# Performance work log

Hardware: AMD Instinct MI355X
Metric: run time of the kernel (lower is better)

The kernel has to match this reference:

```python
import jax, jax.numpy as jnp
import numpy as np

NUM_EMB = 8192
DIM = 64
DECAY = 0.99
EPS = 1e-05
COMMIT = 0.25


def setup_inputs() -> dict:
    key = jax.random.key(0)
    k1, k2, k3 = jax.random.split(key, 3)
    inputs = jax.random.normal(k1, (8, 4096, DIM), jnp.float32)
    weight = jax.random.normal(k2, (NUM_EMB, DIM), jnp.float32)
    ema_cluster_count = jnp.ones((NUM_EMB,), jnp.float32)
    ema_weight_sum = jax.random.normal(k3, (NUM_EMB, DIM), jnp.float32)
    return {
        'inputs': inputs,
        'weight': weight,
        'ema_cluster_count': ema_cluster_count,
        'ema_weight_sum': ema_weight_sum,
    }


def reference(inputs, weight, ema_cluster_count, ema_weight_sum):
    flat = inputs.reshape(-1, DIM)  # [N, D]
    distances = (
        jnp.sum(flat ** 2, axis=1, keepdims=True)
        + jnp.sum(weight ** 2, axis=1)
        - 2.0 * flat @ weight.T
    )
    idx = jnp.argmin(distances, axis=1)  # [N] int

    # EMA stats (training branch): one-hot column sums == segment counts,
    # encodings.T @ flat == segment sums of inputs by code index.
    counts = jax.ops.segment_sum(
        jnp.ones(flat.shape[0], jnp.float32), idx, num_segments=NUM_EMB)
    new_cc = ema_cluster_count * DECAY + (1.0 - DECAY) * counts
    emb_sum = jax.ops.segment_sum(flat, idx, num_segments=NUM_EMB)
    new_ws = ema_weight_sum * DECAY + (1.0 - DECAY) * emb_sum

    n = jnp.sum(new_cc)
    smoothed = (new_cc + EPS) / (n + NUM_EMB * EPS) * n
    new_weight = new_ws / smoothed[:, None]  # updated codebook [K, D]

    quantized_raw = new_weight[idx].reshape(inputs.shape)
    e_latent_loss = jnp.mean((jax.lax.stop_gradient(quantized_raw) - inputs) ** 2)
    vq_loss = COMMIT * e_latent_loss

    avg_probs = counts / flat.shape[0]
    perplexity = jnp.exp(-jnp.sum(avg_probs * jnp.log(avg_probs + 1e-10)))

    # straight-through estimator
    quantized = inputs + jax.lax.stop_gradient(quantized_raw - inputs)
    return quantized, vq_loss, idx, perplexity, new_weight, new_cc, new_ws
```

## Files before the change

kernel.cpp:

```cpp
#include <hip/hip_runtime.h>
#include <math.h>

typedef _Float16 f16x8 __attribute__((ext_vector_type(8)));
typedef float f32x4 __attribute__((ext_vector_type(4)));

#define NROWS 32768
#define KEMB  8192

#define DECAYF 0.99f
#define OMDF   0.01f

#define OUT_Q    0
#define OUT_LOSS 2097152
#define OUT_IDX  2097153
#define OUT_PERP 2129921
#define OUT_NW   2129922
#define OUT_NCC  2654210
#define OUT_NWS  2662402

#define WS_N      0
#define WS_ENT    1
#define WS_COUNTS 4
#define WS_EMB    8196
#define WS_IDX    532484
#define WS_W2H    565252
#define WS_WFRAG  573444
#define WS_ZERO_UNITS 532484

__device__ __forceinline__ float sq_rn(float v) { return __fmul_rn(v, v); }

__device__ __forceinline__ float npsumsq64(const float* vbuf) {
  float a[8];
#pragma unroll
  for (int j = 0; j < 8; ++j) a[j] = sq_rn(vbuf[j]);
#pragma unroll
  for (int m = 1; m < 8; ++m)
#pragma unroll
    for (int j = 0; j < 8; ++j) a[j] = __fadd_rn(a[j], sq_rn(vbuf[m*8 + j]));
  return __fadd_rn(__fadd_rn(__fadd_rn(a[0],a[1]), __fadd_rn(a[2],a[3])),
                   __fadd_rn(__fadd_rn(a[4],a[5]), __fadd_rn(a[6],a[7])));
}

__device__ __forceinline__ void split_f16(float x, _Float16& hi, _Float16& lo) {
  hi = (_Float16)x;
  float r = __fsub_rn(x, (float)hi);
  lo = (_Float16)r;
}

__global__ __launch_bounds__(256) void prep_kernel(const float* __restrict__ wg,
                                                   float* __restrict__ ws) {
  const int tid = blockIdx.x * 256 + threadIdx.x;
  if (tid < KEMB) {
    const float* src = wg + (size_t)tid * 64;
    float vbuf[64];
#pragma unroll
    for (int f = 0; f < 16; ++f) {
      float4 v = *(const float4*)(src + f*4);
      vbuf[f*4+0]=v.x; vbuf[f*4+1]=v.y; vbuf[f*4+2]=v.z; vbuf[f*4+3]=v.w;
    }
    ws[WS_W2H + tid] = __fmul_rn(0.5f, npsumsq64(vbuf));
  } else if (tid < KEMB + 65536) {
    const int u = tid - KEMB;
    const int K = u >> 3, g = u & 7;
    const int n = K & 15, P = K >> 4;
    const int slot = (g&3)*16 + n, shi = g >> 2;
    const float* src = wg + (size_t)K*64 + g*8;
    float4 v0 = *(const float4*)src, v1 = *(const float4*)(src + 4);
    float vv[8] = {v0.x,v0.y,v0.z,v0.w,v1.x,v1.y,v1.z,v1.w};
    f16x8 hi, lo;
#pragma unroll
    for (int j = 0; j < 8; ++j) { _Float16 h, l; split_f16(vv[j], h, l); hi[j]=h; lo[j]=l; }
    _Float16* wf = (_Float16*)(ws + WS_WFRAG);
    *(f16x8*)&wf[((size_t)(P*4 + shi)*64 + slot)*8]     = hi;
    *(f16x8*)&wf[((size_t)(P*4 + 2 + shi)*64 + slot)*8] = lo;
  }
}

#define COMPUTE_PANEL(I, B0, B1, B2, B3, W2)                                        \
  {                                                                                 \
    const f32x4 cin = {(W2), (W2), (W2), (W2)};                                     \
    f32x4 acc[2];                                                                   \
    _Pragma("unroll")                                                               \
    for (int rt = 0; rt < 2; ++rt) acc[rt] = __builtin_amdgcn_mfma_f32_16x16x32_f16(a[rt][0], (B0), cin, 0,0,0); \
    _Pragma("unroll")                                                               \
    for (int rt = 0; rt < 2; ++rt) acc[rt] = __builtin_amdgcn_mfma_f32_16x16x32_f16(a[rt][1], (B1), acc[rt], 0,0,0); \
    _Pragma("unroll")                                                               \
    for (int rt = 0; rt < 2; ++rt) acc[rt] = __builtin_amdgcn_mfma_f32_16x16x32_f16(a[rt][2], (B0), acc[rt], 0,0,0); \
    _Pragma("unroll")                                                               \
    for (int rt = 0; rt < 2; ++rt) acc[rt] = __builtin_amdgcn_mfma_f32_16x16x32_f16(a[rt][3], (B1), acc[rt], 0,0,0); \
    _Pragma("unroll")                                                               \
    for (int rt = 0; rt < 2; ++rt) acc[rt] = __builtin_amdgcn_mfma_f32_16x16x32_f16(a[rt][0], (B2), acc[rt], 0,0,0); \
    _Pragma("unroll")                                                               \
    for (int rt = 0; rt < 2; ++rt) acc[rt] = __builtin_amdgcn_mfma_f32_16x16x32_f16(a[rt][1], (B3), acc[rt], 0,0,0); \
    const int kk = (I)*64 + cg*16 + n16;                                            \
    _Pragma("unroll")                                                               \
    for (int rt = 0; rt < 2; ++rt)                                                  \
      _Pragma("unroll")                                                             \
      for (int reg = 0; reg < 4; ++reg) {                                           \
        const float dist = acc[rt][reg];                                            \
        const int bi = rt*4 + reg;                                                  \
        if (dist < best[bi]) { best[bi] = dist; bestk[bi] = kk; }                   \
      }                                                                             \
  }

#define LOADB(I, C0, C1, C2, C3, CW)                                                \
  {                                                                                 \
    const size_t base = ((size_t)((I)*4 + cg) * 256) * 8 + lane8;                   \
    C0 = *(const f16x8*)&wfrag[base];                                               \
    C1 = *(const f16x8*)&wfrag[base + 512];                                         \
    C2 = *(const f16x8*)&wfrag[base + 1024];                                        \
    C3 = *(const f16x8*)&wfrag[base + 1536];                                        \
    CW = w2hg[(I)*64 + cg*16 + n16];                                                \
  }

__global__ __launch_bounds__(1024) void argmin_kernel(const float* __restrict__ xg,
                                                      float* __restrict__ out,
                                                      float* __restrict__ ws) {
  __shared__ __align__(16) _Float16 xp[8*4*64*8];
  __shared__ float md[128*4];
  __shared__ int   mk[128*4];
  __shared__ int   bkL[128];

  const int t    = threadIdx.x;
  const int lane = t & 63, wv = t >> 6;
  const int quad = lane >> 4, n16 = lane & 15;
  const int rg = wv >> 2, cg = wv & 3;
  const int row0 = blockIdx.x * 128;
  const _Float16* __restrict__ wfrag = (const _Float16*)(ws + WS_WFRAG);
  const float* __restrict__ w2hg = ws + WS_W2H;

  {
    const int u  = t;
    const int rp = u >> 7, n = (u >> 3) & 15, g = u & 7;
    const float* src = xg + (size_t)(row0 + rp*16 + n)*64 + g*8;
    float4 v0 = *(const float4*)src, v1 = *(const float4*)(src + 4);
    float vv[8] = {v0.x,v0.y,v0.z,v0.w,v1.x,v1.y,v1.z,v1.w};
    f16x8 hi, lo;
#pragma unroll
    for (int j = 0; j < 8; ++j) { _Float16 h, l; split_f16(-vv[j], h, l); hi[j]=h; lo[j]=l; }
    const int slot = (g&3)*16 + n, shi = g >> 2;
    *(f16x8*)&xp[(((rp*4) + shi)*64 + slot)*8]     = hi;
    *(f16x8*)&xp[(((rp*4) + 2 + shi)*64 + slot)*8] = lo;
  }
  __syncthreads();

  f16x8 a[2][4];
#pragma unroll
  for (int rt = 0; rt < 2; ++rt)
#pragma unroll
    for (int s = 0; s < 4; ++s)
      a[rt][s] = *(const f16x8*)&xp[(((rg*2+rt)*4 + s)*64 + lane)*8];

  float best[8]; int bestk[8];
#pragma unroll
  for (int i = 0; i < 8; ++i) { best[i] = INFINITY; bestk[i] = 0; }

  const size_t lane8 = (size_t)lane * 8;
  f16x8 p0, p1, p2, p3, q0, q1, q2, q3;
  float pw, qw;
  LOADB(0, p0, p1, p2, p3, pw);

  for (int it = 0; it < 128; it += 2) {
    LOADB(it+1, q0, q1, q2, q3, qw);
    COMPUTE_PANEL(it, p0, p1, p2, p3, pw);
    if (it + 2 < 128) LOADB(it+2, p0, p1, p2, p3, pw);
    COMPUTE_PANEL(it+1, q0, q1, q2, q3, qw);
  }

#pragma unroll
  for (int bi = 0; bi < 8; ++bi) {
    float bd = best[bi]; int bk = bestk[bi];
#pragma unroll
    for (int m = 1; m < 16; m <<= 1) {
      const float od = __shfl_xor(bd, m, 64);
      const int   ok = __shfl_xor(bk, m, 64);
      if (od < bd || (od == bd && ok < bk)) { bd = od; bk = ok; }
    }
    best[bi] = bd; bestk[bi] = bk;
  }
  if (n16 == 0) {
#pragma unroll
    for (int rt = 0; rt < 2; ++rt)
#pragma unroll
      for (int reg = 0; reg < 4; ++reg) {
        const int row = rg*32 + rt*16 + quad*4 + reg;
        md[row*4 + cg] = best[rt*4+reg];
        mk[row*4 + cg] = bestk[rt*4+reg];
      }
  }
  __syncthreads();

  if (t < 128) {
    const int row = t;
    float bd = md[row*4]; int bk = mk[row*4];
#pragma unroll
    for (int u = 1; u < 4; ++u) {
      const float d2 = md[row*4 + u]; const int k2 = mk[row*4 + u];
      if (d2 < bd || (d2 == bd && k2 < bk)) { bd = d2; bk = k2; }
    }
    out[OUT_IDX + row0 + row] = (float)bk;
    ((int*)ws)[WS_IDX + row0 + row] = bk;
    bkL[row] = bk;
    atomicAdd(&ws[WS_COUNTS + bk], 1.0f);
  }
  __syncthreads();

#pragma unroll 4
  for (int r = 0; r < 8; ++r) {
    const int row = wv*8 + r;
    const int k = bkL[row];
    atomicAdd(&ws[WS_EMB + (size_t)k*64 + lane],
              xg[(size_t)(row0 + row)*64 + lane]);
  }
}

__global__ __launch_bounds__(256) void stats_kernel(const float* __restrict__ cc,
                                                    float* __restrict__ out,
                                                    float* __restrict__ ws) {
  const int t = threadIdx.x;
  float v1 = 0.0f, v2 = 0.0f;
#pragma unroll
  for (int i = 0; i < 32; ++i) {
    const int k = i*256 + t;
    const float cnt = ws[WS_COUNTS + k];
    const float ncc = __fadd_rn(__fmul_rn(DECAYF, cc[k]), __fmul_rn(OMDF, cnt));
    out[OUT_NCC + k] = ncc;
    const float p = cnt * (1.0f/32768.0f);
    v1 += ncc;
    v2 += __fmul_rn(p, logf(__fadd_rn(p, 1e-10f)));
  }
#pragma unroll
  for (int off = 32; off > 0; off >>= 1) {
    v1 += __shfl_down(v1, off);
    v2 += __shfl_down(v2, off);
  }
  __shared__ float s1[4], s2[4];
  const int lane = t & 63, wid = t >> 6;
  if (lane == 0) { s1[wid] = v1; s2[wid] = v2; }
  __syncthreads();
  if (t == 0) {
    ws[WS_N]   = (s1[0]+s1[1]) + (s1[2]+s1[3]);
    ws[WS_ENT] = (s2[0]+s2[1]) + (s2[2]+s2[3]);
  }
}

__global__ __launch_bounds__(256) void update_kernel(const float* __restrict__ ws0,
                                                     float* __restrict__ out,
                                                     float* __restrict__ ws) {
  const int e4 = blockIdx.x * 256 + threadIdx.x;
  const int k = e4 >> 4;
  const float n = ws[WS_N];
  const float ncc = out[OUT_NCC + k];
  const float smoothed = __fmul_rn(__fadd_rn(ncc, 1e-5f) / __fadd_rn(n, 0.08192f), n);
  float4 w0 = *(const float4*)(ws0 + (size_t)e4*4);
  float4 em = *(const float4*)(ws + WS_EMB + (size_t)e4*4);
  float wv[4] = {w0.x, w0.y, w0.z, w0.w};
  float ev[4] = {em.x, em.y, em.z, em.w};
  float nwsv[4], nwv[4];
#pragma unroll
  for (int i = 0; i < 4; ++i) {
    nwsv[i] = __fadd_rn(__fmul_rn(DECAYF, wv[i]), __fmul_rn(OMDF, ev[i]));
    nwv[i]  = nwsv[i] / smoothed;
  }
  float4 onws = {nwsv[0], nwsv[1], nwsv[2], nwsv[3]};
  float4 onw  = {nwv[0],  nwv[1],  nwv[2],  nwv[3]};
  *(float4*)(out + OUT_NWS + (size_t)e4*4) = onws;
  *(float4*)(out + OUT_NW  + (size_t)e4*4) = onw;
  if (e4 == 0) out[OUT_PERP] = expf(-ws[WS_ENT]);
}

__global__ __launch_bounds__(256) void quant_kernel(const float* __restrict__ xg,
                                                    float* __restrict__ out,
                                                    float* __restrict__ ws) {
  const int t = threadIdx.x;
  const int* idxb = (const int*)ws + WS_IDX;
  float v = 0.0f;
#pragma unroll
  for (int j = 0; j < 4; ++j) {
    const int e4 = (j*512 + blockIdx.x)*256 + t;
    const int row = e4 >> 4, d = (e4 & 15) * 4;
    const int k = idxb[row];
    const float* nw = out + OUT_NW + (size_t)k*64 + d;
    float2 q0 = *(const float2*)nw, q1 = *(const float2*)(nw + 2);
    float4 x = *(const float4*)(xg + (size_t)e4*4);
    float qv[4] = {q0.x, q0.y, q1.x, q1.y};
    float xv[4] = {x.x, x.y, x.z, x.w};
    float4 o;
    float ov[4];
#pragma unroll
    for (int i = 0; i < 4; ++i) {
      const float df = __fsub_rn(qv[i], xv[i]);
      ov[i] = __fadd_rn(xv[i], df);
      v = fmaf(df, df, v);
    }
    o.x = ov[0]; o.y = ov[1]; o.z = ov[2]; o.w = ov[3];
    *(float4*)(out + OUT_Q + (size_t)e4*4) = o;
  }
#pragma unroll
  for (int off = 32; off > 0; off >>= 1) v += __shfl_down(v, off);
  __shared__ float sm[4];
  const int lane = t & 63, wid = t >> 6;
  if (lane == 0) sm[wid] = v;
  __syncthreads();
  if (t == 0) ws[WS_COUNTS + blockIdx.x] = (sm[0]+sm[1]) + (sm[2]+sm[3]);
}

__global__ void final_kernel(float* __restrict__ out, const float* __restrict__ ws) {
  const int t = threadIdx.x;
  float v = 0.0f;
#pragma unroll
  for (int i = 0; i < 8; ++i) v += ws[WS_COUNTS + i*64 + t];
#pragma unroll
  for (int off = 32; off > 0; off >>= 1) v += __shfl_down(v, off);
  if (t == 0) out[OUT_LOSS] = __fmul_rn(0.25f, v / 2097152.0f);
}

extern "C" void kernel_launch(void* const* d_in, const int* in_sizes, int n_in,
                              void* d_out, int out_size, void* d_ws, size_t ws_size,
                              hipStream_t stream) {
  (void)in_sizes; (void)n_in; (void)out_size; (void)ws_size;
  const float* x   = (const float*)d_in[0];
  const float* w   = (const float*)d_in[1];
  const float* cc  = (const float*)d_in[2];
  const float* ws0 = (const float*)d_in[3];
  float* out = (float*)d_out;
  float* ws  = (float*)d_ws;

  hipMemsetAsync(d_ws, 0, (size_t)WS_ZERO_UNITS * 4, stream);
  hipLaunchKernelGGL(prep_kernel,   dim3(288),  dim3(256),  0, stream, w, ws);
  hipLaunchKernelGGL(argmin_kernel, dim3(256),  dim3(1024), 0, stream, x, out, ws);
  hipLaunchKernelGGL(stats_kernel,  dim3(1),    dim3(256),  0, stream, cc, out, ws);
  hipLaunchKernelGGL(update_kernel, dim3(512),  dim3(256),  0, stream, ws0, out, ws);
  hipLaunchKernelGGL(quant_kernel,  dim3(512),  dim3(256),  0, stream, x, out, ws);
  hipLaunchKernelGGL(final_kernel,  dim3(1),    dim3(64),   0, stream, out, ws);
}
```

Before: 202.9 us.

## Switch argmin to 32x32x16 MFMA tiles with 512-thread blocks, fold memset into prep

Reorganizes the codebook and input fragment layouts for 32x32x16 f16 MFMA. Each wave now computes 64 rows by 32 codes per panel, with 8-wave blocks and two blocks per CU. This reduces B-fragment loads and per-instruction overhead relative to the 16x16 tiles. The workspace memset is folded into prep_kernel to remove a separate launch, and stats_kernel uses 1024 threads. More accumulator and best/bestk registers per thread raise register pressure.

```diff
diff --git a/kernel.cpp b/kernel.cpp
--- a/kernel.cpp
+++ b/kernel.cpp
@@ -3,6 +3,7 @@
 
 typedef _Float16 f16x8 __attribute__((ext_vector_type(8)));
 typedef float f32x4 __attribute__((ext_vector_type(4)));
+typedef float f32x16 __attribute__((ext_vector_type(16)));
 
 #define NROWS 32768
 #define KEMB  8192
@@ -50,6 +51,7 @@
 __global__ __launch_bounds__(256) void prep_kernel(const float* __restrict__ wg,
                                                    float* __restrict__ ws) {
   const int tid = blockIdx.x * 256 + threadIdx.x;
+  for (int i = tid; i < WS_ZERO_UNITS; i += 73728) ws[i] = 0.0f;
   if (tid < KEMB) {
     const float* src = wg + (size_t)tid * 64;
     float vbuf[64];
@@ -59,133 +61,148 @@
       vbuf[f*4+0]=v.x; vbuf[f*4+1]=v.y; vbuf[f*4+2]=v.z; vbuf[f*4+3]=v.w;
     }
     ws[WS_W2H + tid] = __fmul_rn(0.5f, npsumsq64(vbuf));
-  } else if (tid < KEMB + 65536) {
+  } else {
     const int u = tid - KEMB;
     const int K = u >> 3, g = u & 7;
-    const int n = K & 15, P = K >> 4;
-    const int slot = (g&3)*16 + n, shi = g >> 2;
+    const int P = K >> 5, col = K & 31;
+    const int c = g >> 1, h = g & 1;
+    const int lane_t = col + 32*h;
     const float* src = wg + (size_t)K*64 + g*8;
     float4 v0 = *(const float4*)src, v1 = *(const float4*)(src + 4);
     float vv[8] = {v0.x,v0.y,v0.z,v0.w,v1.x,v1.y,v1.z,v1.w};
     f16x8 hi, lo;
 #pragma unroll
-    for (int j = 0; j < 8; ++j) { _Float16 h, l; split_f16(vv[j], h, l); hi[j]=h; lo[j]=l; }
+    for (int j = 0; j < 8; ++j) { _Float16 hh, ll; split_f16(vv[j], hh, ll); hi[j]=hh; lo[j]=ll; }
     _Float16* wf = (_Float16*)(ws + WS_WFRAG);
-    *(f16x8*)&wf[((size_t)(P*4 + shi)*64 + slot)*8]     = hi;
-    *(f16x8*)&wf[((size_t)(P*4 + 2 + shi)*64 + slot)*8] = lo;
-  }
-}
-
-#define COMPUTE_PANEL(I, B0, B1, B2, B3, W2)                                        \
-  {                                                                                 \
-    const f32x4 cin = {(W2), (W2), (W2), (W2)};                                     \
-    f32x4 acc[2];                                                                   \
-    _Pragma("unroll")                                                               \
-    for (int rt = 0; rt < 2; ++rt) acc[rt] = __builtin_amdgcn_mfma_f32_16x16x32_f16(a[rt][0], (B0), cin, 0,0,0); \
-    _Pragma("unroll")                                                               \
-    for (int rt = 0; rt < 2; ++rt) acc[rt] = __builtin_amdgcn_mfma_f32_16x16x32_f16(a[rt][1], (B1), acc[rt], 0,0,0); \
-    _Pragma("unroll")                                                               \
-    for (int rt = 0; rt < 2; ++rt) acc[rt] = __builtin_amdgcn_mfma_f32_16x16x32_f16(a[rt][2], (B0), acc[rt], 0,0,0); \
-    _Pragma("unroll")                                                               \
-    for (int rt = 0; rt < 2; ++rt) acc[rt] = __builtin_amdgcn_mfma_f32_16x16x32_f16(a[rt][3], (B1), acc[rt], 0,0,0); \
-    _Pragma("unroll")                                                               \
-    for (int rt = 0; rt < 2; ++rt) acc[rt] = __builtin_amdgcn_mfma_f32_16x16x32_f16(a[rt][0], (B2), acc[rt], 0,0,0); \
-    _Pragma("unroll")                                                               \
-    for (int rt = 0; rt < 2; ++rt) acc[rt] = __builtin_amdgcn_mfma_f32_16x16x32_f16(a[rt][1], (B3), acc[rt], 0,0,0); \
-    const int kk = (I)*64 + cg*16 + n16;                                            \
-    _Pragma("unroll")                                                               \
-    for (int rt = 0; rt < 2; ++rt)                                                  \
-      _Pragma("unroll")                                                             \
-      for (int reg = 0; reg < 4; ++reg) {                                           \
-        const float dist = acc[rt][reg];                                            \
-        const int bi = rt*4 + reg;                                                  \
-        if (dist < best[bi]) { best[bi] = dist; bestk[bi] = kk; }                   \
-      }                                                                             \
-  }
-
-#define LOADB(I, C0, C1, C2, C3, CW)                                                \
-  {                                                                                 \
-    const size_t base = ((size_t)((I)*4 + cg) * 256) * 8 + lane8;                   \
-    C0 = *(const f16x8*)&wfrag[base];                                               \
-    C1 = *(const f16x8*)&wfrag[base + 512];                                         \
-    C2 = *(const f16x8*)&wfrag[base + 1024];                                        \
-    C3 = *(const f16x8*)&wfrag[base + 1536];                                        \
-    CW = w2hg[(I)*64 + cg*16 + n16];                                                \
-  }
-
-__global__ __launch_bounds__(1024) void argmin_kernel(const float* __restrict__ xg,
-                                                      float* __restrict__ out,
-                                                      float* __restrict__ ws) {
-  __shared__ __align__(16) _Float16 xp[8*4*64*8];
+    *(f16x8*)&wf[((size_t)(P*8 + c)    *64 + lane_t)*8] = hi;
+    *(f16x8*)&wf[((size_t)(P*8 + c + 4)*64 + lane_t)*8] = lo;
+  }
+}
+
+__global__ __launch_bounds__(512, 2) void argmin_kernel(const float* __restrict__ xg,
+                                                        float* __restrict__ out,
+                                                        float* __restrict__ ws) {
+  __shared__ __align__(16) _Float16 xp[4*8*64*8];
   __shared__ float md[128*4];
   __shared__ int   mk[128*4];
   __shared__ int   bkL[128];
 
   const int t    = threadIdx.x;
   const int lane = t & 63, wv = t >> 6;
-  const int quad = lane >> 4, n16 = lane & 15;
+  const int col = lane & 31, half = lane >> 5;
   const int rg = wv >> 2, cg = wv & 3;
   const int row0 = blockIdx.x * 128;
   const _Float16* __restrict__ wfrag = (const _Float16*)(ws + WS_WFRAG);
   const float* __restrict__ w2hg = ws + WS_W2H;
 
-  {
-    const int u  = t;
-    const int rp = u >> 7, n = (u >> 3) & 15, g = u & 7;
-    const float* src = xg + (size_t)(row0 + rp*16 + n)*64 + g*8;
+#pragma unroll
+  for (int it = 0; it < 2; ++it) {
+    const int u  = t + 512*it;
+    const int r = u >> 3, g = u & 7;
+    const int rp = r >> 5, c = g >> 1, h = g & 1;
+    const int lane_t = (r & 31) + 32*h;
+    const float* src = xg + (size_t)(row0 + r)*64 + g*8;
     float4 v0 = *(const float4*)src, v1 = *(const float4*)(src + 4);
     float vv[8] = {v0.x,v0.y,v0.z,v0.w,v1.x,v1.y,v1.z,v1.w};
     f16x8 hi, lo;
 #pragma unroll
-    for (int j = 0; j < 8; ++j) { _Float16 h, l; split_f16(-vv[j], h, l); hi[j]=h; lo[j]=l; }
-    const int slot = (g&3)*16 + n, shi = g >> 2;
-    *(f16x8*)&xp[(((rp*4) + shi)*64 + slot)*8]     = hi;
-    *(f16x8*)&xp[(((rp*4) + 2 + shi)*64 + slot)*8] = lo;
-  }
-  __syncthreads();
-
-  f16x8 a[2][4];
+    for (int j = 0; j < 8; ++j) { _Float16 hh, ll; split_f16(-vv[j], hh, ll); hi[j]=hh; lo[j]=ll; }
+    *(f16x8*)&xp[(((rp*8) + c)    *64 + lane_t)*8] = hi;
+    *(f16x8*)&xp[(((rp*8) + c + 4)*64 + lane_t)*8] = lo;
+  }
+  __syncthreads();
+
+  f16x8 a[2][8];
 #pragma unroll
   for (int rt = 0; rt < 2; ++rt)
 #pragma unroll
-    for (int s = 0; s < 4; ++s)
-      a[rt][s] = *(const f16x8*)&xp[(((rg*2+rt)*4 + s)*64 + lane)*8];
-
-  float best[8]; int bestk[8];
-#pragma unroll
-  for (int i = 0; i < 8; ++i) { best[i] = INFINITY; bestk[i] = 0; }
+    for (int c = 0; c < 8; ++c)
+      a[rt][c] = *(const f16x8*)&xp[(((rg*2+rt)*8 + c)*64 + lane)*8];
+
+  float best[32]; int bestk[32];
+#pragma unroll
+  for (int i = 0; i < 32; ++i) { best[i] = INFINITY; bestk[i] = 0; }
 
   const size_t lane8 = (size_t)lane * 8;
-  f16x8 p0, p1, p2, p3, q0, q1, q2, q3;
+
+#define LOADB32(P, B, CW)                                                    \
+  {                                                                          \
+    const size_t base = (size_t)(P)*4096 + lane8;                            \
+    _Pragma("unroll")                                                        \
+    for (int c = 0; c < 8; ++c) B[c] = *(const f16x8*)&wfrag[base + c*512];  \
+    CW = w2hg[(P)*32 + col];                                                 \
+  }
+
+#define COMPUTE32(P, B, W2)                                                  \
+  {                                                                          \
+    f32x16 cin;                                                              \
+    _Pragma("unroll")                                                        \
+    for (int i = 0; i < 16; ++i) cin[i] = (W2);                              \
+    f32x16 ac0, ac1;                                                         \
+    ac0 = __builtin_amdgcn_mfma_f32_32x32x16_f16(a[0][0], B[0], cin, 0,0,0); \
+    ac1 = __builtin_amdgcn_mfma_f32_32x32x16_f16(a[1][0], B[0], cin, 0,0,0); \
+    ac0 = __builtin_amdgcn_mfma_f32_32x32x16_f16(a[0][1], B[1], ac0, 0,0,0); \
+    ac1 = __builtin_amdgcn_mfma_f32_32x32x16_f16(a[1][1], B[1], ac1, 0,0,0); \
+    ac0 = __builtin_amdgcn_mfma_f32_32x32x16_f16(a[0][2], B[2], ac0, 0,0,0); \
+    ac1 = __builtin_amdgcn_mfma_f32_32x32x16_f16(a[1][2], B[2], ac1, 0,0,0); \
+    ac0 = __builtin_amdgcn_mfma_f32_32x32x16_f16(a[0][3], B[3], ac0, 0,0,0); \
+    ac1 = __builtin_amdgcn_mfma_f32_32x32x16_f16(a[1][3], B[3], ac1, 0,0,0); \
+    ac0 = __builtin_amdgcn_mfma_f32_32x32x16_f16(a[0][0], B[4], ac0, 0,0,0); \
+    ac1 = __builtin_amdgcn_mfma_f32_32x32x16_f16(a[1][0], B[4], ac1, 0,0,0); \
+    ac0 = __builtin_amdgcn_mfma_f32_32x32x16_f16(a[0][1], B[5], ac0, 0,0,0); \
+    ac1 = __builtin_amdgcn_mfma_f32_32x32x16_f16(a[1][1], B[5], ac1, 0,0,0); \
+    ac0 = __builtin_amdgcn_mfma_f32_32x32x16_f16(a[0][2], B[6], ac0, 0,0,0); \
+    ac1 = __builtin_amdgcn_mfma_f32_32x32x16_f16(a[1][2], B[6], ac1, 0,0,0); \
+    ac0 = __builtin_amdgcn_mfma_f32_32x32x16_f16(a[0][3], B[7], ac0, 0,0,0); \
+    ac1 = __builtin_amdgcn_mfma_f32_32x32x16_f16(a[1][3], B[7], ac1, 0,0,0); \
+    ac0 = __builtin_amdgcn_mfma_f32_32x32x16_f16(a[0][4], B[0], ac0, 0,0,0); \
+    ac1 = __builtin_amdgcn_mfma_f32_32x32x16_f16(a[1][4], B[0], ac1, 0,0,0); \
+    ac0 = __builtin_amdgcn_mfma_f32_32x32x16_f16(a[0][5], B[1], ac0, 0,0,0); \
+    ac1 = __builtin_amdgcn_mfma_f32_32x32x16_f16(a[1][5], B[1], ac1, 0,0,0); \
+    ac0 = __builtin_amdgcn_mfma_f32_32x32x16_f16(a[0][6], B[2], ac0, 0,0,0); \
+    ac1 = __builtin_amdgcn_mfma_f32_32x32x16_f16(a[1][6], B[2], ac1, 0,0,0); \
+    ac0 = __builtin_amdgcn_mfma_f32_32x32x16_f16(a[0][7], B[3], ac0, 0,0,0); \
+    ac1 = __builtin_amdgcn_mfma_f32_32x32x16_f16(a[1][7], B[3], ac1, 0,0,0); \
+    const int kk = (P)*32 + col;                                             \
+    _Pragma("unroll")                                                        \
+    for (int reg = 0; reg < 16; ++reg) {                                     \
+      const float d0 = ac0[reg];                                             \
+      if (d0 < best[reg])      { best[reg] = d0;      bestk[reg] = kk; }     \
+      const float d1 = ac1[reg];                                             \
+      if (d1 < best[16+reg])   { best[16+reg] = d1;   bestk[16+reg] = kk; }  \
+    }                                                                        \
+  }
+
+  f16x8 bp[8], bq[8];
   float pw, qw;
-  LOADB(0, p0, p1, p2, p3, pw);
-
-  for (int it = 0; it < 128; it += 2) {
-    LOADB(it+1, q0, q1, q2, q3, qw);
-    COMPUTE_PANEL(it, p0, p1, p2, p3, pw);
-    if (it + 2 < 128) LOADB(it+2, p0, p1, p2, p3, pw);
-    COMPUTE_PANEL(it+1, q0, q1, q2, q3, qw);
-  }
-
-#pragma unroll
-  for (int bi = 0; bi < 8; ++bi) {
+  LOADB32(cg, bp, pw);
+
+  for (int it = 0; it < 64; it += 2) {
+    LOADB32((it+1)*4 + cg, bq, qw);
+    COMPUTE32(it*4 + cg, bp, pw);
+    if (it + 2 < 64) LOADB32((it+2)*4 + cg, bp, pw);
+    COMPUTE32((it+1)*4 + cg, bq, qw);
+  }
+
+#pragma unroll
+  for (int bi = 0; bi < 32; ++bi) {
     float bd = best[bi]; int bk = bestk[bi];
 #pragma unroll
-    for (int m = 1; m < 16; m <<= 1) {
+    for (int m = 1; m < 32; m <<= 1) {
       const float od = __shfl_xor(bd, m, 64);
       const int   ok = __shfl_xor(bk, m, 64);
       if (od < bd || (od == bd && ok < bk)) { bd = od; bk = ok; }
     }
     best[bi] = bd; bestk[bi] = bk;
   }
-  if (n16 == 0) {
+  if (col == 0) {
 #pragma unroll
     for (int rt = 0; rt < 2; ++rt)
 #pragma unroll
-      for (int reg = 0; reg < 4; ++reg) {
-        const int row = rg*32 + rt*16 + quad*4 + reg;
-        md[row*4 + cg] = best[rt*4+reg];
-        mk[row*4 + cg] = bestk[rt*4+reg];
+      for (int reg = 0; reg < 16; ++reg) {
+        const int row = rg*64 + rt*32 + (reg & 3) + 8*(reg >> 2) + 4*half;
+        md[row*4 + cg] = best[rt*16 + reg];
+        mk[row*4 + cg] = bestk[rt*16 + reg];
       }
   }
   __syncthreads();
@@ -206,22 +223,22 @@
   __syncthreads();
 
 #pragma unroll 4
-  for (int r = 0; r < 8; ++r) {
-    const int row = wv*8 + r;
+  for (int r = 0; r < 16; ++r) {
+    const int row = wv*16 + r;
     const int k = bkL[row];
     atomicAdd(&ws[WS_EMB + (size_t)k*64 + lane],
               xg[(size_t)(row0 + row)*64 + lane]);
   }
 }
 
-__global__ __launch_bounds__(256) void stats_kernel(const float* __restrict__ cc,
-                                                    float* __restrict__ out,
-                                                    float* __restrict__ ws) {
+__global__ __launch_bounds__(1024) void stats_kernel(const float* __restrict__ cc,
+                                                     float* __restrict__ out,
+                                                     float* __restrict__ ws) {
   const int t = threadIdx.x;
   float v1 = 0.0f, v2 = 0.0f;
 #pragma unroll
-  for (int i = 0; i < 32; ++i) {
-    const int k = i*256 + t;
+  for (int i = 0; i < 8; ++i) {
+    const int k = i*1024 + t;
     const float cnt = ws[WS_COUNTS + k];
     const float ncc = __fadd_rn(__fmul_rn(DECAYF, cc[k]), __fmul_rn(OMDF, cnt));
     out[OUT_NCC + k] = ncc;
@@ -234,13 +251,15 @@
     v1 += __shfl_down(v1, off);
     v2 += __shfl_down(v2, off);
   }
-  __shared__ float s1[4], s2[4];
+  __shared__ float s1[16], s2[16];
   const int lane = t & 63, wid = t >> 6;
   if (lane == 0) { s1[wid] = v1; s2[wid] = v2; }
   __syncthreads();
   if (t == 0) {
-    ws[WS_N]   = (s1[0]+s1[1]) + (s1[2]+s1[3]);
-    ws[WS_ENT] = (s2[0]+s2[1]) + (s2[2]+s2[3]);
+    float n = 0.0f, e = 0.0f;
+#pragma unroll
+    for (int i = 0; i < 16; ++i) { n += s1[i]; e += s2[i]; }
+    ws[WS_N] = n; ws[WS_ENT] = e;
   }
 }
 
@@ -326,10 +345,9 @@
   float* out = (float*)d_out;
   float* ws  = (float*)d_ws;
 
-  hipMemsetAsync(d_ws, 0, (size_t)WS_ZERO_UNITS * 4, stream);
   hipLaunchKernelGGL(prep_kernel,   dim3(288),  dim3(256),  0, stream, w, ws);
-  hipLaunchKernelGGL(argmin_kernel, dim3(256),  dim3(1024), 0, stream, x, out, ws);
-  hipLaunchKernelGGL(stats_kernel,  dim3(1),    dim3(256),  0, stream, cc, out, ws);
+  hipLaunchKernelGGL(argmin_kernel, dim3(256),  dim3(512),  0, stream, x, out, ws);
+  hipLaunchKernelGGL(stats_kernel,  dim3(1),    dim3(1024), 0, stream, cc, out, ws);
   hipLaunchKernelGGL(update_kernel, dim3(512),  dim3(256),  0, stream, ws0, out, ws);
   hipLaunchKernelGGL(quant_kernel,  dim3(512),  dim3(256),  0, stream, x, out, ws);
   hipLaunchKernelGGL(final_kernel,  dim3(1),    dim3(64),   0, stream, out, ws);
```

After: 207.8 us. +2.4%, slower.
